# Optimization experiments

Measured on AMD Instinct MI355X. Metric: run time of the kernel, lower is better.

The kernel has to match this reference:

```python
import jax, jax.numpy as jnp
import numpy as np

N = 100000      # nodes
E = 1600000     # edges (before self loops)
IN_F = 128
OUT_F = 32
HEADS = 4
NEG_SLOPE = 0.2


def setup_inputs() -> dict:
    key = jax.random.key(0)
    k1, k2, k3, k4, k5, k6 = jax.random.split(key, 6)
    x = jax.random.normal(k1, (N, IN_F), dtype=jnp.float32)
    edge_index = jax.random.randint(k2, (2, E), 0, N, dtype=jnp.int64)
    # PyG GATConv params: shared linear W [in, H*F], attention vectors att_src/att_dst [1,H,F], bias [H*F]
    glorot = (6.0 / (IN_F + HEADS * OUT_F)) ** 0.5
    W = jax.random.uniform(k3, (IN_F, HEADS * OUT_F), dtype=jnp.float32, minval=-glorot, maxval=glorot)
    ga = (6.0 / (1 + OUT_F)) ** 0.5
    att_src = jax.random.uniform(k4, (HEADS, OUT_F), dtype=jnp.float32, minval=-ga, maxval=ga)
    att_dst = jax.random.uniform(k5, (HEADS, OUT_F), dtype=jnp.float32, minval=-ga, maxval=ga)
    bias = jnp.zeros((HEADS * OUT_F,), dtype=jnp.float32)
    return {"x": x, "edge_index": edge_index, "W": W, "att_src": att_src, "att_dst": att_dst, "bias": bias}


def reference(x, edge_index, W, att_src, att_dst, bias):
    n = x.shape[0]
    # add self loops (PyG add_self_loops=True)
    loops = jnp.arange(n, dtype=edge_index.dtype)
    src = jnp.concatenate([edge_index[0], loops])  # [E+N] message source j
    dst = jnp.concatenate([edge_index[1], loops])  # [E+N] message target i

    h = (x @ W).reshape(n, HEADS, OUT_F)                 # [N,H,F]
    a_src = jnp.sum(h * att_src[None], axis=-1)          # [N,H]
    a_dst = jnp.sum(h * att_dst[None], axis=-1)          # [N,H]

    e = a_src[src] + a_dst[dst]                          # [E',H]
    e = jax.nn.leaky_relu(e, NEG_SLOPE)
    # per-destination softmax over incoming edges
    m = jax.ops.segment_max(e, dst, num_segments=n)      # [N,H]
    ex = jnp.exp(e - m[dst])
    s = jax.ops.segment_sum(ex, dst, num_segments=n)     # [N,H]
    alpha = ex / (s[dst] + 1e-16)                        # [E',H]

    msg = h[src] * alpha[:, :, None]                     # [E',H,F]
    out = jax.ops.segment_sum(msg, dst, num_segments=n)  # [N,H,F]
    return out.reshape(n, HEADS * OUT_F) + bias
```

## Files before the change

### kernel.cpp

```cpp
#include <hip/hip_runtime.h>


#define NEG_SLOPE 0.2f
#define NB_MAX 256
#define BSHIFT 9
#define CHUNK 4096
#define CAP 11264

typedef __attribute__((ext_vector_type(8))) short short8;
typedef __attribute__((ext_vector_type(4))) float f32x4;

__device__ __forceinline__ unsigned int rne16(unsigned int u) {
  return (u + 0x7fffu + ((u >> 16) & 1u)) >> 16;
}
__device__ __forceinline__ unsigned int f2bf_pack(float a, float b) {
  return (rne16(__float_as_uint(b)) << 16) | (rne16(__float_as_uint(a)) & 0xffffu);
}

__global__ __launch_bounds__(256) void k_hist_prep(
    const int* __restrict__ ei, int* __restrict__ bucketCnt, int E,
    const float* __restrict__ W, unsigned short* __restrict__ Wt, int nbBin) {
  __shared__ int h[NB_MAX];
  int tid = threadIdx.x;
  if ((int)blockIdx.x >= nbBin) {
    int idx = (blockIdx.x - nbBin) * 256 + tid;
    int k = idx >> 7, col = idx & 127;
    Wt[col * 128 + k] = (unsigned short)rne16(__float_as_uint(W[idx]));
    return;
  }
  h[tid] = 0;
  __syncthreads();
  int base = blockIdx.x * CHUNK;
  int n = E - base; if (n > CHUNK) n = CHUNK;
  for (int i = tid; i < n; i += 256) atomicAdd(&h[ei[E + base + i] >> BSHIFT], 1);
  __syncthreads();
  if (h[tid]) atomicAdd(&bucketCnt[tid], h[tid]);
}

__global__ void k_bucket_scan(const int* __restrict__ bucketCnt,
                              int* __restrict__ bucketOff, int* __restrict__ bcur) {
  int lane = threadIdx.x;
  int base = lane * 4;
  int v0 = bucketCnt[base], v1 = bucketCnt[base + 1];
  int v2 = bucketCnt[base + 2], v3 = bucketCnt[base + 3];
  int s = v0 + v1 + v2 + v3;
  int inc = s;
#pragma unroll
  for (int d = 1; d < 64; d <<= 1) {
    int t = __shfl_up(inc, d, 64);
    if (lane >= d) inc += t;
  }
  int ex = inc - s;
  bucketOff[base] = ex;          bcur[base] = ex;
  bucketOff[base + 1] = ex + v0; bcur[base + 1] = ex + v0;
  bucketOff[base + 2] = ex + v0 + v1; bcur[base + 2] = ex + v0 + v1;
  bucketOff[base + 3] = ex + v0 + v1 + v2; bcur[base + 3] = ex + v0 + v1 + v2;
  if (lane == 63) bucketOff[256] = inc;
}

__global__ __launch_bounds__(256) void k_binmm(
    const int* __restrict__ ei, int* __restrict__ bcur,
    unsigned int* __restrict__ binned, int E, int nb, int nbBin,
    const float* __restrict__ x, const unsigned short* __restrict__ Wt,
    unsigned int* __restrict__ hb,
    const float* __restrict__ attS, const float* __restrict__ attD,
    float* __restrict__ aS, float* __restrict__ aD, int Nn) {
  __shared__ uint2 buf[CHUNK];
  __shared__ int hist[NB_MAX];
  __shared__ int loc[NB_MAX];
  __shared__ int gbase[NB_MAX];
  int tid = threadIdx.x;

  if ((int)blockIdx.x < nbBin) {
    int e0 = blockIdx.x * CHUNK;
    int n = E - e0; if (n > CHUNK) n = CHUNK;

    for (int i = tid; i < NB_MAX; i += 256) hist[i] = 0;
    __syncthreads();

    int dstv[CHUNK / 256];
    int rankv[CHUNK / 256];
#pragma unroll
    for (int j = 0; j < CHUNK / 256; ++j) {
      int idx = j * 256 + tid;
      dstv[j] = -1;
      if (idx < n) {
        int d = ei[E + e0 + idx];
        dstv[j] = d;
        rankv[j] = atomicAdd(&hist[d >> BSHIFT], 1);
      }
    }
    __syncthreads();

    if (tid < 64) {
      int base = tid * 4;
      int v0 = hist[base], v1 = hist[base + 1], v2 = hist[base + 2], v3 = hist[base + 3];
      int s = v0 + v1 + v2 + v3;
      int inc = s;
#pragma unroll
      for (int d = 1; d < 64; d <<= 1) {
        int t = __shfl_up(inc, d, 64);
        if (tid >= d) inc += t;
      }
      int ex = inc - s;
      loc[base] = ex; loc[base + 1] = ex + v0;
      loc[base + 2] = ex + v0 + v1; loc[base + 3] = ex + v0 + v1 + v2;
    }
    __syncthreads();

#pragma unroll
    for (int j = 0; j < CHUNK / 256; ++j) {
      if (dstv[j] >= 0) {
        int s = ei[e0 + j * 256 + tid];
        int b = dstv[j] >> BSHIFT;
        buf[loc[b] + rankv[j]] = make_uint2((unsigned)s, (unsigned)dstv[j]);
      }
    }
    for (int b = tid; b < nb; b += 256)
      if (hist[b] > 0) gbase[b] = atomicAdd(&bcur[b], hist[b]);
    __syncthreads();

    for (int s = tid; s < n; s += 256) {
      uint2 p = buf[s];
      int b = (int)(p.y >> BSHIFT);
      binned[gbase[b] + (s - loc[b])] = p.x | ((p.y & 511u) << 20);
    }
    return;
  }

  int gbid = blockIdx.x - nbBin;
  int w = tid >> 6, lane = tid & 63;
  int m = lane & 15, q = lane >> 4;
  int r0 = gbid * 64 + w * 16;
  int rowA = r0 + m; if (rowA >= Nn) rowA = Nn - 1;
  const float* xrow = x + (unsigned)rowA * 128u;

  f32x4 acc[8];
#pragma unroll
  for (int t = 0; t < 8; ++t) acc[t] = (f32x4){0.f, 0.f, 0.f, 0.f};

#pragma unroll
  for (int ks = 0; ks < 4; ++ks) {
    int k0 = ks * 32 + q * 8;
    float4 a0 = *(const float4*)(xrow + k0);
    float4 a1 = *(const float4*)(xrow + k0 + 4);
    unsigned au[4];
    au[0] = f2bf_pack(a0.x, a0.y);
    au[1] = f2bf_pack(a0.z, a0.w);
    au[2] = f2bf_pack(a1.x, a1.y);
    au[3] = f2bf_pack(a1.z, a1.w);
    short8 af = *(short8*)au;
#pragma unroll
    for (int t = 0; t < 8; ++t) {
      short8 bf = *(const short8*)(Wt + (unsigned)(t * 16 + m) * 128u + k0);
      acc[t] = __builtin_amdgcn_mfma_f32_16x16x32_bf16(af, bf, acc[t], 0, 0, 0);
    }
  }

  float sSa[4], sSb[4], sDa[4], sDb[4];
#pragma unroll
  for (int u = 0; u < 4; ++u) {
    sSa[u] = attS[u * 32 + m]; sSb[u] = attS[u * 32 + m + 16];
    sDa[u] = attD[u * 32 + m]; sDb[u] = attD[u * 32 + m + 16];
  }

#pragma unroll
  for (int r = 0; r < 4; ++r) {
    int rowo = r0 + q * 4 + r;
    bool ok = rowo < Nn;
    if (ok) {
#pragma unroll
      for (int u = 0; u < 4; ++u)
        hb[(unsigned)rowo * 64u + u * 16 + m] = f2bf_pack(acc[2 * u][r], acc[2 * u + 1][r]);
    }
#pragma unroll
    for (int u = 0; u < 4; ++u) {
      float pS = acc[2 * u][r] * sSa[u] + acc[2 * u + 1][r] * sSb[u];
      float pD = acc[2 * u][r] * sDa[u] + acc[2 * u + 1][r] * sDb[u];
#pragma unroll
      for (int d = 8; d >= 1; d >>= 1) {
        pS += __shfl_down(pS, d, 16);
        pD += __shfl_down(pD, d, 16);
      }
      if (ok && m == 0) {
        aS[(unsigned)rowo * 4u + u] = pS;
        aD[(unsigned)rowo * 4u + u] = pD;
      }
    }
  }
}

__global__ __launch_bounds__(256) void k_scatter2(
    const unsigned int* __restrict__ binned, const int* __restrict__ bucketOff,
    int* __restrict__ off, int* __restrict__ ssrc, int Nn, int E, int nb) {
  __shared__ int cnt[512];
  __shared__ int loc[512];
  __shared__ int obuf[CAP];
  __shared__ int wsum[4];
  int b = blockIdx.x, tid = threadIdx.x;
  int node0 = b << BSHIFT;
  int nnodes = Nn - node0; if (nnodes > 512) nnodes = 512;
  int base = bucketOff[b];
  int nE = bucketOff[b + 1] - base;

  cnt[tid] = 0; cnt[tid + 256] = 0;
  __syncthreads();
  for (int i = tid; i < nE; i += 256)
    atomicAdd(&cnt[(binned[base + i] >> 20) & 511u], 1);
  __syncthreads();

  int i0 = 2 * tid, i1 = 2 * tid + 1;
  int v0 = cnt[i0] + (i0 < nnodes ? 1 : 0);
  int v1 = cnt[i1] + (i1 < nnodes ? 1 : 0);
  int s = v0 + v1;
  int lane = tid & 63, w = tid >> 6;
  int inc = s;
#pragma unroll
  for (int d = 1; d < 64; d <<= 1) {
    int t = __shfl_up(inc, d, 64);
    if (lane >= d) inc += t;
  }
  if (lane == 63) wsum[w] = inc;
  __syncthreads();
  int wbase = 0;
  for (int ww = 0; ww < w; ++ww) wbase += wsum[ww];
  int ex = wbase + inc - s;
  loc[i0] = ex; loc[i1] = ex + v0;
  __syncthreads();

  int csrBase = base + node0;
  for (int i = tid; i < nnodes; i += 256) {
    int l = loc[i];
    off[node0 + i] = csrBase + l;
    obuf[l] = node0 + i;
  }
  for (int i = tid; i < 512; i += 256) cnt[i] = loc[i] + 1;
  __syncthreads();

  for (int i = tid; i < nE; i += 256) {
    unsigned p = binned[base + i];
    int d = (p >> 20) & 511u;
    int pos = atomicAdd(&cnt[d], 1);
    if (pos < CAP) obuf[pos] = (int)(p & 0xFFFFFu);
  }
  __syncthreads();

  int tot = nE + nnodes;
  for (int i = tid; i < tot; i += 256) ssrc[csrBase + i] = obuf[i];
  if (b == nb - 1 && tid == 0) off[Nn] = E + Nn;
}

__global__ __launch_bounds__(256) void k_aggregate(
    const unsigned int* __restrict__ hb, const float* __restrict__ aS, const float* __restrict__ aD,
    const int* __restrict__ off, const int* __restrict__ ssrc,
    const float* __restrict__ bias, float* __restrict__ out, int Nn) {
  int wave = threadIdx.x >> 6;
  int lane = threadIdx.x & 63;
  int node = blockIdx.x * 4 + wave;
  if (node >= Nn) return;
  int un = __builtin_amdgcn_readfirstlane(node);
  unsigned hd = (unsigned)lane >> 4;
  float ad = aD[(unsigned)un * 4u + hd];
  int p0 = off[un], p1 = off[un + 1];
  const int* sp = ssrc + p0;
  int deg = p1 - p0;
  int nch = deg >> 2;
  float accx = 0.f, accy = 0.f, den = 0.f;

  for (int c = 0; c < nch; ++c) {
    int s0 = sp[0], s1 = sp[1], s2 = sp[2], s3 = sp[3];
    unsigned v0 = hb[(unsigned)s0 * 64u + lane];
    unsigned v1 = hb[(unsigned)s1 * 64u + lane];
    unsigned v2 = hb[(unsigned)s2 * 64u + lane];
    unsigned v3 = hb[(unsigned)s3 * 64u + lane];
    float e0 = aS[(unsigned)s0 * 4u + hd] + ad;
    float e1 = aS[(unsigned)s1 * 4u + hd] + ad;
    float e2 = aS[(unsigned)s2 * 4u + hd] + ad;
    float e3 = aS[(unsigned)s3 * 4u + hd] + ad;
    e0 = e0 > 0.f ? e0 : NEG_SLOPE * e0;
    e1 = e1 > 0.f ? e1 : NEG_SLOPE * e1;
    e2 = e2 > 0.f ? e2 : NEG_SLOPE * e2;
    e3 = e3 > 0.f ? e3 : NEG_SLOPE * e3;
    float ex0 = __expf(e0), ex1 = __expf(e1), ex2 = __expf(e2), ex3 = __expf(e3);
    den += ((ex0 + ex1) + (ex2 + ex3));
    accx += ex0 * __uint_as_float(v0 << 16);
    accy += ex0 * __uint_as_float(v0 & 0xffff0000u);
    accx += ex1 * __uint_as_float(v1 << 16);
    accy += ex1 * __uint_as_float(v1 & 0xffff0000u);
    accx += ex2 * __uint_as_float(v2 << 16);
    accy += ex2 * __uint_as_float(v2 & 0xffff0000u);
    accx += ex3 * __uint_as_float(v3 << 16);
    accy += ex3 * __uint_as_float(v3 & 0xffff0000u);
    sp += 4;
  }
  for (int p = nch << 2; p < deg; ++p) {
    int src = (ssrc + p0)[p];
    float e = aS[(unsigned)src * 4u + hd] + ad;
    e = e > 0.f ? e : NEG_SLOPE * e;
    float ex = __expf(e);
    unsigned v = hb[(unsigned)src * 64u + lane];
    accx += ex * __uint_as_float(v << 16);
    accy += ex * __uint_as_float(v & 0xffff0000u);
    den += ex;
  }
  float inv = 1.0f / (den + 1e-16f);
  unsigned col = hd * 32u + ((unsigned)lane & 15u);
  out[(unsigned)un * 128u + col] = accx * inv + bias[col];
  out[(unsigned)un * 128u + col + 16u] = accy * inv + bias[col + 16];
}

extern "C" void kernel_launch(void* const* d_in, const int* in_sizes, int n_in,
                              void* d_out, int out_size, void* d_ws, size_t ws_size,
                              hipStream_t stream) {
  const float* x    = (const float*)d_in[0];
  const int*   ei   = (const int*)d_in[1];
  const float* W    = (const float*)d_in[2];
  const float* attS = (const float*)d_in[3];
  const float* attD = (const float*)d_in[4];
  const float* bias = (const float*)d_in[5];
  float* out = (float*)d_out;

  const int Nn = in_sizes[0] / 128;
  const int E  = in_sizes[1] / 2;
  const int nb = (Nn + (1 << BSHIFT) - 1) >> BSHIFT;
  const int nbBin = (E + CHUNK - 1) / CHUNK;
  const int nGemm = (Nn + 63) / 64;

  char* ws = (char*)d_ws;
  size_t o = 0;
  auto take = [&](size_t bytes) { void* p = ws + o; o += (bytes + 255) & ~(size_t)255; return p; };
  int* off       = (int*)take((size_t)(Nn + 1) * 4);
  int* ssrc      = (int*)take((size_t)(E + Nn) * 4);
  int* bucketCnt = (int*)take((size_t)NB_MAX * 4);
  int* bucketOff = (int*)take((size_t)(NB_MAX + 1) * 4);
  int* bcur      = (int*)take((size_t)NB_MAX * 4);
  float* aS      = (float*)take((size_t)Nn * 4 * 4);
  float* aD      = (float*)take((size_t)Nn * 4 * 4);
  unsigned short* Wt = (unsigned short*)take((size_t)128 * 128 * 2);
  unsigned int* hb = (unsigned int*)take((size_t)Nn * 64 * 4);
  unsigned int* binned = (unsigned int*)take((size_t)E * 4);
  (void)ws_size; (void)o;

  hipMemsetAsync(bucketCnt, 0, NB_MAX * 4, stream);
  k_hist_prep<<<nbBin + 64, 256, 0, stream>>>(ei, bucketCnt, E, W, Wt, nbBin);
  k_bucket_scan<<<1, 64, 0, stream>>>(bucketCnt, bucketOff, bcur);
  k_binmm<<<nbBin + nGemm, 256, 0, stream>>>(ei, bcur, binned, E, nb, nbBin,
                                             x, Wt, hb, attS, attD, aS, aD, Nn);
  k_scatter2<<<nb, 256, 0, stream>>>(binned, bucketOff, off, ssrc, Nn, E, nb);
  k_aggregate<<<(Nn + 3) / 4, 256, 0, stream>>>(hb, aS, aD, off, ssrc, bias, out, Nn);
}
```

Baseline: 252.4 us.

## Software-pipeline aggregate gathers, prescale logits for exp2, and compact bin staging buffer

The aggregate loop now issues the next four neighbours' feature and attention loads before it computes the current group, so gather latency overlaps the math. Attention logits are multiplied by log2(e) in the GEMM epilogue, which lets exp2f replace __expf. LeakyReLU becomes fmaxf, and accumulation uses packed f32x2 FMAs with two denominator sums. The binning kernel stores pre-packed 32-bit entries plus a byte bucket id in shared memory instead of uint2, which roughly halves LDS traffic; the cost is extra registers for the prefetched values.

```diff
diff --git a/kernel.cpp b/kernel.cpp
--- a/kernel.cpp
+++ b/kernel.cpp
@@ -6,9 +6,11 @@
 #define BSHIFT 9
 #define CHUNK 4096
 #define CAP 11264
+#define LOG2E 1.4426950408889634f
 
 typedef __attribute__((ext_vector_type(8))) short short8;
 typedef __attribute__((ext_vector_type(4))) float f32x4;
+typedef __attribute__((ext_vector_type(2))) float f32x2;
 
 __device__ __forceinline__ unsigned int rne16(unsigned int u) {
   return (u + 0x7fffu + ((u >> 16) & 1u)) >> 16;
@@ -65,7 +67,8 @@
     unsigned int* __restrict__ hb,
     const float* __restrict__ attS, const float* __restrict__ attD,
     float* __restrict__ aS, float* __restrict__ aD, int Nn) {
-  __shared__ uint2 buf[CHUNK];
+  __shared__ unsigned int buf[CHUNK];
+  __shared__ unsigned char bkt[CHUNK];
   __shared__ int hist[NB_MAX];
   __shared__ int loc[NB_MAX];
   __shared__ int gbase[NB_MAX];
@@ -111,9 +114,11 @@
 #pragma unroll
     for (int j = 0; j < CHUNK / 256; ++j) {
       if (dstv[j] >= 0) {
-        int s = ei[e0 + j * 256 + tid];
+        int src = ei[e0 + j * 256 + tid];
         int b = dstv[j] >> BSHIFT;
-        buf[loc[b] + rankv[j]] = make_uint2((unsigned)s, (unsigned)dstv[j]);
+        int slot = loc[b] + rankv[j];
+        buf[slot] = (unsigned)src | ((unsigned)(dstv[j] & 511) << 20);
+        bkt[slot] = (unsigned char)b;
       }
     }
     for (int b = tid; b < nb; b += 256)
@@ -121,9 +126,8 @@
     __syncthreads();
 
     for (int s = tid; s < n; s += 256) {
-      uint2 p = buf[s];
-      int b = (int)(p.y >> BSHIFT);
-      binned[gbase[b] + (s - loc[b])] = p.x | ((p.y & 511u) << 20);
+      int b = bkt[s];
+      binned[gbase[b] + (s - loc[b])] = buf[s];
     }
     return;
   }
@@ -183,8 +187,8 @@
         pD += __shfl_down(pD, d, 16);
       }
       if (ok && m == 0) {
-        aS[(unsigned)rowo * 4u + u] = pS;
-        aD[(unsigned)rowo * 4u + u] = pD;
+        aS[(unsigned)rowo * 4u + u] = pS * LOG2E;
+        aD[(unsigned)rowo * 4u + u] = pD * LOG2E;
       }
     }
   }
@@ -265,48 +269,63 @@
   const int* sp = ssrc + p0;
   int deg = p1 - p0;
   int nch = deg >> 2;
-  float accx = 0.f, accy = 0.f, den = 0.f;
-
+  f32x2 acc = {0.f, 0.f};
+  float denA = 0.f, denB = 0.f;
+
+  int s0 = 0, s1 = 0, s2 = 0, s3 = 0;
+  unsigned v0 = 0, v1 = 0, v2 = 0, v3 = 0;
+  float a0 = 0.f, a1 = 0.f, a2 = 0.f, a3 = 0.f;
+  if (nch > 0) {
+    s0 = sp[0]; s1 = sp[1]; s2 = sp[2]; s3 = sp[3];
+    v0 = hb[(unsigned)s0 * 64u + lane]; v1 = hb[(unsigned)s1 * 64u + lane];
+    v2 = hb[(unsigned)s2 * 64u + lane]; v3 = hb[(unsigned)s3 * 64u + lane];
+    a0 = aS[(unsigned)s0 * 4u + hd]; a1 = aS[(unsigned)s1 * 4u + hd];
+    a2 = aS[(unsigned)s2 * 4u + hd]; a3 = aS[(unsigned)s3 * 4u + hd];
+    sp += 4;
+  }
   for (int c = 0; c < nch; ++c) {
-    int s0 = sp[0], s1 = sp[1], s2 = sp[2], s3 = sp[3];
-    unsigned v0 = hb[(unsigned)s0 * 64u + lane];
-    unsigned v1 = hb[(unsigned)s1 * 64u + lane];
-    unsigned v2 = hb[(unsigned)s2 * 64u + lane];
-    unsigned v3 = hb[(unsigned)s3 * 64u + lane];
-    float e0 = aS[(unsigned)s0 * 4u + hd] + ad;
-    float e1 = aS[(unsigned)s1 * 4u + hd] + ad;
-    float e2 = aS[(unsigned)s2 * 4u + hd] + ad;
-    float e3 = aS[(unsigned)s3 * 4u + hd] + ad;
-    e0 = e0 > 0.f ? e0 : NEG_SLOPE * e0;
-    e1 = e1 > 0.f ? e1 : NEG_SLOPE * e1;
-    e2 = e2 > 0.f ? e2 : NEG_SLOPE * e2;
-    e3 = e3 > 0.f ? e3 : NEG_SLOPE * e3;
-    float ex0 = __expf(e0), ex1 = __expf(e1), ex2 = __expf(e2), ex3 = __expf(e3);
-    den += ((ex0 + ex1) + (ex2 + ex3));
-    accx += ex0 * __uint_as_float(v0 << 16);
-    accy += ex0 * __uint_as_float(v0 & 0xffff0000u);
-    accx += ex1 * __uint_as_float(v1 << 16);
-    accy += ex1 * __uint_as_float(v1 & 0xffff0000u);
-    accx += ex2 * __uint_as_float(v2 << 16);
-    accy += ex2 * __uint_as_float(v2 & 0xffff0000u);
-    accx += ex3 * __uint_as_float(v3 << 16);
-    accy += ex3 * __uint_as_float(v3 & 0xffff0000u);
-    sp += 4;
+    int t0 = 0, t1 = 0, t2 = 0, t3 = 0;
+    unsigned w0 = 0, w1 = 0, w2 = 0, w3 = 0;
+    float b0 = 0.f, b1 = 0.f, b2 = 0.f, b3 = 0.f;
+    if (c + 1 < nch) {
+      t0 = sp[0]; t1 = sp[1]; t2 = sp[2]; t3 = sp[3];
+      w0 = hb[(unsigned)t0 * 64u + lane]; w1 = hb[(unsigned)t1 * 64u + lane];
+      w2 = hb[(unsigned)t2 * 64u + lane]; w3 = hb[(unsigned)t3 * 64u + lane];
+      b0 = aS[(unsigned)t0 * 4u + hd]; b1 = aS[(unsigned)t1 * 4u + hd];
+      b2 = aS[(unsigned)t2 * 4u + hd]; b3 = aS[(unsigned)t3 * 4u + hd];
+      sp += 4;
+    }
+    float e0 = a0 + ad, e1 = a1 + ad, e2 = a2 + ad, e3 = a3 + ad;
+    e0 = fmaxf(e0, NEG_SLOPE * e0); e1 = fmaxf(e1, NEG_SLOPE * e1);
+    e2 = fmaxf(e2, NEG_SLOPE * e2); e3 = fmaxf(e3, NEG_SLOPE * e3);
+    float x0 = exp2f(e0), x1 = exp2f(e1), x2 = exp2f(e2), x3 = exp2f(e3);
+    denA += x0 + x1; denB += x2 + x3;
+    f32x2 h0 = { __uint_as_float(v0 << 16), __uint_as_float(v0 & 0xffff0000u) };
+    f32x2 h1 = { __uint_as_float(v1 << 16), __uint_as_float(v1 & 0xffff0000u) };
+    f32x2 h2 = { __uint_as_float(v2 << 16), __uint_as_float(v2 & 0xffff0000u) };
+    f32x2 h3 = { __uint_as_float(v3 << 16), __uint_as_float(v3 & 0xffff0000u) };
+    acc = h0 * x0 + acc;
+    acc = h1 * x1 + acc;
+    acc = h2 * x2 + acc;
+    acc = h3 * x3 + acc;
+    s0 = t0; s1 = t1; s2 = t2; s3 = t3;
+    v0 = w0; v1 = w1; v2 = w2; v3 = w3;
+    a0 = b0; a1 = b1; a2 = b2; a3 = b3;
   }
   for (int p = nch << 2; p < deg; ++p) {
     int src = (ssrc + p0)[p];
     float e = aS[(unsigned)src * 4u + hd] + ad;
-    e = e > 0.f ? e : NEG_SLOPE * e;
-    float ex = __expf(e);
+    e = fmaxf(e, NEG_SLOPE * e);
+    float ex = exp2f(e);
     unsigned v = hb[(unsigned)src * 64u + lane];
-    accx += ex * __uint_as_float(v << 16);
-    accy += ex * __uint_as_float(v & 0xffff0000u);
-    den += ex;
-  }
-  float inv = 1.0f / (den + 1e-16f);
+    f32x2 hh = { __uint_as_float(v << 16), __uint_as_float(v & 0xffff0000u) };
+    acc = hh * ex + acc;
+    denA += ex;
+  }
+  float inv = 1.0f / (denA + denB + 1e-16f);
   unsigned col = hd * 32u + ((unsigned)lane & 15u);
-  out[(unsigned)un * 128u + col] = accx * inv + bias[col];
-  out[(unsigned)un * 128u + col + 16u] = accy * inv + bias[col + 16];
+  out[(unsigned)un * 128u + col] = acc.x * inv + bias[col];
+  out[(unsigned)un * 128u + col + 16u] = acc.y * inv + bias[col + 16];
 }
 
 extern "C" void kernel_launch(void* const* d_in, const int* in_sizes, int n_in,
```

Result: no change. 251.3 us (-0.4%).
